# Kernel optimization log

Hardware: AMD Instinct MI355X
Metric: run time of the kernel (lower is better)

Reference implementation:

```python
import math
import jax, jax.numpy as jnp
import numpy as np

B, L, H, D = 1, 2048, 16, 64
M = 24            # nb_features
WINDOW = 128      # local_context / window_size
SCALE = 0.125     # softmax_scale = 1/sqrt(D)
MASK_VAL = -10000.0
EPS = 1e-4        # SBPerformerFeatures eps


def setup_inputs() -> dict:
    key = jax.random.key(0)
    k1, k2 = jax.random.split(key)
    qkv = jax.random.normal(k1, (B, L, 3, H, D), dtype=jnp.float32)
    proj = jax.random.normal(k2, (M, D), dtype=jnp.float32)  # Performer random features
    return {"qkv": qkv, "proj": proj}


def _performer_features(x, proj, is_query):
    # Softmax-kernel random features with separate log scale (scatterbrain SBPerformerFeatures).
    # exp(t*q.k) ~= exp(q_log + k_log) * <q_prime, k_prime>
    dn = math.sqrt(SCALE)
    xs = x * dn                                            # (b,h,l,d)
    x_dash = jnp.einsum('bhld,md->bhlm', xs, proj)         # (b,h,l,m)
    x_norm = 0.5 * jnp.sum(xs * xs, axis=-1, keepdims=True)
    half_log_m = 0.5 * math.log(M)
    if is_query:
        stab = jax.lax.stop_gradient(jnp.max(x_dash, axis=-1, keepdims=True))
        prime = jnp.exp(x_dash - stab) + EPS               # per-row stabilized
        log_scale = stab - x_norm - half_log_m             # (b,h,l,1)
    else:
        stab = jax.lax.stop_gradient(jnp.max(x_dash, axis=(-1, -2), keepdims=True))
        prime = jnp.exp(x_dash - x_norm - stab) + EPS      # norm folded in (needed for cumsum)
        log_scale = stab - half_log_m                      # (b,h,1,1)
    return prime, log_scale


def _band_mask(n):
    idx = jnp.arange(n)
    diff = idx[:, None] - idx[None, :]                     # i - j
    return jnp.where((diff >= 0) & (diff <= WINDOW), 0.0, MASK_VAL)  # (L,L)


def _forward(qkv, proj):
    q, k, v = qkv[:, :, 0], qkv[:, :, 1], qkv[:, :, 2]     # (b,l,h,d)
    q = jnp.transpose(q, (0, 2, 1, 3))                     # (b,h,l,d)
    k = jnp.transpose(k, (0, 2, 1, 3))
    v = jnp.transpose(v, (0, 2, 1, 3))

    # --- GlobalPerformer path ---
    q_prime, q_log = _performer_features(q, proj, True)    # (b,h,l,m), (b,h,l,1)
    k_prime, k_log = _performer_features(k, proj, False)   # (b,h,l,m), (b,h,1,1)
    global_scale = q_log + k_log                           # (b,h,l,1)

    k_cum = jnp.cumsum(k_prime, axis=2)
    global_out_cumsum = jnp.einsum('bhlm,bhlm->bhl', q_prime, k_cum)
    # causal_dot_product: out_i = q'_i . sum_{j<=i} k'_j v_j^T
    kv = jnp.cumsum(k_prime[..., :, None] * v[..., None, :], axis=2)   # (b,h,l,m,d)
    global_out = jnp.einsum('bhlm,bhlmd->bhld', q_prime, kv)

    mask = _band_mask(L)
    p_scores = jnp.einsum('bhme,bhne->bhmn', q_prime, k_prime) * SCALE
    global_qk = jnp.maximum(p_scores + mask[None, None], 0.0)  # masked_fill(<=0, 0)

    # --- Local exact softmax path ---
    scores = jnp.einsum('bhme,bhne->bhmn', q, k) * SCALE
    local_qk = scores + mask[None, None]
    qk_lse = jax.scipy.special.logsumexp(local_qk, axis=-1, keepdims=True)  # (b,h,l,1)

    gqk_sum = jnp.sum(global_qk, axis=-1, keepdims=True)
    global_log_norm = jnp.log(jnp.maximum(global_out_cumsum[..., None] - gqk_sum, 1e-24)) + global_scale
    log_norm = jnp.logaddexp(qk_lse, global_log_norm)      # (b,h,l,1)
    global_prime_scale = jnp.exp(global_scale - log_norm)  # (b,h,l,1)

    local_score = jax.nn.softmax(local_qk - log_norm, axis=-1) - global_qk * global_prime_scale
    out = jnp.einsum('bhmn,bhnd->bhmd', local_score, v) + global_out * global_prime_scale
    return jnp.transpose(out, (0, 2, 1, 3))                # (b,l,h,d)


def reference(qkv, proj):
    return _forward(qkv, proj)
```

## Files before the change

### kernel.cpp

```cpp
#include <hip/hip_runtime.h>
#include <hip/hip_bf16.h>

#define L_SEQ 2048
#define NH 16
#define DH 64
#define NCH 32
#define SCALE_F 0.125f
#define EPS_F 1e-4f
#define DN_F 0.35355339059327373f
#define HLM_F 1.5890269151739727f

typedef __attribute__((ext_vector_type(8))) short short8v;
typedef __attribute__((ext_vector_type(4))) float f32x4;

__device__ __forceinline__ unsigned short f2bf(float x) {
  unsigned u = __float_as_uint(x);
  u += 0x7FFFu + ((u >> 16) & 1u);
  return (unsigned short)(u >> 16);
}
__device__ __forceinline__ unsigned pk2(float a, float b) {
  return (unsigned)f2bf(a) | ((unsigned)f2bf(b) << 16);
}
__device__ __forceinline__ float stab_from_pmax(const float* __restrict__ pmax, int h, int t) {
  float v = pmax[h * 32 + (t & 31)];
  v = fmaxf(v, __shfl_xor(v, 1));  v = fmaxf(v, __shfl_xor(v, 2));
  v = fmaxf(v, __shfl_xor(v, 4));  v = fmaxf(v, __shfl_xor(v, 8));
  v = fmaxf(v, __shfl_xor(v, 16));
  return v;
}

__global__ __launch_bounds__(256) void k1_feat(
    const float* __restrict__ qkv, const float* __restrict__ proj,
    float* __restrict__ kdash, float* __restrict__ knorm,
    float* __restrict__ qdash, float* __restrict__ qnorm,
    float* __restrict__ pmax, unsigned* __restrict__ kbw, unsigned* __restrict__ qbw)
{
  __shared__ __attribute__((aligned(16))) float sP[24][68];
  __shared__ __attribute__((aligned(16))) float sX[64][68];
  __shared__ float sRed[256];
  const int c = blockIdx.x, h = blockIdx.y, qk = blockIdx.z, t = threadIdx.x;
  const int slot = qk ? 0 : 1;
  for (int i = t; i < 24 * 64; i += 256) sP[i >> 6][i & 63] = proj[i];
  for (int i = t; i < 1024; i += 256) {
    int rr = i >> 4, d4 = (i & 15) * 4;
    int l = c * 64 + rr;
    *(float4*)&sX[rr][d4] = *(const float4*)(qkv + (((size_t)l * 3 + slot) * NH + h) * DH + d4);
  }
  __syncthreads();
  unsigned* dstw = qk ? qbw : kbw;
  for (int w = t; w < 2048; w += 256) {
    int rr = w >> 5, wo = w & 31;
    int l = c * 64 + rr;
    float2 xv = *(const float2*)&sX[rr][2 * wo];
    dstw[((size_t)h * L_SEQ + l) * 32 + (wo ^ ((rr & 7) << 2))] = pk2(xv.x, xv.y);
  }
  const int r = t >> 2, mg = t & 3;
  float acc[6] = {0.f, 0.f, 0.f, 0.f, 0.f, 0.f};
  float sq = 0.f;
  for (int d4 = 0; d4 < 16; ++d4) {
    float4 xv = *(const float4*)&sX[r][d4 * 4];
    sq += xv.x * xv.x; sq += xv.y * xv.y; sq += xv.z * xv.z; sq += xv.w * xv.w;
#pragma unroll
    for (int i = 0; i < 6; ++i) {
      float4 pv = *(const float4*)&sP[mg * 6 + i][d4 * 4];
      acc[i] += xv.x * pv.x; acc[i] += xv.y * pv.y;
      acc[i] += xv.z * pv.z; acc[i] += xv.w * pv.w;
    }
  }
  int l = c * 64 + r;
  float* dsh = qk ? qdash : kdash;
  float lmax = -1e30f;
#pragma unroll
  for (int i = 0; i < 6; ++i) {
    float v = acc[i] * DN_F;
    dsh[((size_t)h * L_SEQ + l) * 24 + mg * 6 + i] = v;
    lmax = fmaxf(lmax, v);
  }
  if (mg == 0) (qk ? qnorm : knorm)[h * L_SEQ + l] = 0.5f * SCALE_F * sq;
  if (qk == 0) {
    sRed[t] = lmax;
    __syncthreads();
#pragma unroll
    for (int s = 128; s > 0; s >>= 1) {
      if (t < s) sRed[t] = fmaxf(sRed[t], sRed[t + s]);
      __syncthreads();
    }
    if (t == 0) pmax[h * 32 + c] = sRed[0];
  }
}

__global__ __launch_bounds__(256) void k3_kprime(
    const float* __restrict__ qkv, const float* __restrict__ kdash,
    const float* __restrict__ knorm, const float* __restrict__ pmax,
    unsigned* __restrict__ kpw, float* __restrict__ kpfx, float* __restrict__ kvs,
    unsigned* __restrict__ vtw)
{
  __shared__ float sKp[64][25];
  __shared__ __attribute__((aligned(16))) float sV[64][68];
  const int c = blockIdx.x, h = blockIdx.y, t = threadIdx.x;
  const float stab = stab_from_pmax(pmax, h, t);
  for (int i = t; i < 1024; i += 256) {
    int rr = i >> 4, d4 = (i & 15) * 4;
    int l = c * 64 + rr;
    *(float4*)&sV[rr][d4] = *(const float4*)(qkv + (((size_t)l * 3 + 2) * NH + h) * DH + d4);
  }
  for (int i = t; i < 1536; i += 256) {
    int r = i / 24, m = i % 24;
    int l = c * 64 + r;
    sKp[r][m] = __expf(kdash[((size_t)h * L_SEQ + l) * 24 + m] - knorm[h * L_SEQ + l] - stab) + EPS_F;
  }
  __syncthreads();
  for (int w = t; w < 1024; w += 256) {
    int r = w >> 4, wo = w & 15;
    int l = c * 64 + r;
    float a = (wo < 12) ? sKp[r][2 * wo] : 0.f;
    float bb = (wo < 12) ? sKp[r][2 * wo + 1] : 0.f;
    kpw[((size_t)h * L_SEQ + l) * 16 + (wo ^ ((r & 3) << 2))] = pk2(a, bb);
  }
  for (int w = t; w < 2048; w += 256) {
    int d = w >> 5, jp = w & 31;
    vtw[((size_t)h * NCH + c) * 2048 + d * 32 + (jp ^ ((d & 7) << 2))] = pk2(sV[2 * jp][d], sV[2 * jp + 1][d]);
  }
  if (t < 192) {
    const int m = t % 24, dO = (t / 24) * 8;
    float a0x = 0.f, a0y = 0.f, a0z = 0.f, a0w = 0.f;
    float a1x = 0.f, a1y = 0.f, a1z = 0.f, a1w = 0.f;
    for (int r2 = 0; r2 < 64; ++r2) {
      float kp = sKp[r2][m];
      float4 v0 = *(const float4*)&sV[r2][dO];
      float4 v1 = *(const float4*)&sV[r2][dO + 4];
      a0x += kp * v0.x; a0y += kp * v0.y; a0z += kp * v0.z; a0w += kp * v0.w;
      a1x += kp * v1.x; a1y += kp * v1.y; a1z += kp * v1.z; a1w += kp * v1.w;
    }
    float* dst = kvs + ((size_t)h * NCH + c) * 1536 + m * 64 + dO;
    float4 o0 = {a0x, a0y, a0z, a0w};
    float4 o1 = {a1x, a1y, a1z, a1w};
    *(float4*)dst = o0;
    *(float4*)(dst + 4) = o1;
  } else if (t < 216) {
    const int m = t - 192;
    float run = 0.f;
    for (int r2 = 0; r2 < 64; ++r2) {
      run += sKp[r2][m];
      kpfx[((size_t)h * L_SEQ + c * 64 + r2) * 24 + m] = run;
    }
  }
}

__global__ __launch_bounds__(256, 2) void k6_attn(
    const unsigned* __restrict__ kpw, const float* __restrict__ kpfx,
    const float* __restrict__ kvs, const unsigned* __restrict__ vtw,
    const float* __restrict__ qdash, const float* __restrict__ qnorm,
    const float* __restrict__ pmax, const unsigned* __restrict__ kbw,
    const unsigned* __restrict__ qbw, float* __restrict__ out)
{
  __shared__ __attribute__((aligned(16))) char lds[80736];
  char* sKW = lds;
  char* sKp = lds + 24576;
  char* sV  = lds + 36864;
  char* sQ  = lds + 61440;
  char* sQp = lds + 69632;
  float* sSum = (float*)(lds + 73728);
  float* sGps = sSum + 64;
  float* sRin = sGps + 64;
  float* sKcx = (float*)(lds + 74496);
  float* sPfx = (float*)(lds + 74592);

  const int b = blockIdx.x, h = blockIdx.y, t = threadIdx.x;
  const int wv = t >> 6, lane = t & 63, g = lane >> 4, ln = lane & 15;
  const int keybase = b * 64 - 128;
  const int jmin = (b >= 2) ? 0 : (128 - 64 * b);
  const int rA = wv * 16 + ln;

  for (int w = t; w < 1536; w += 256) {
    int r = w >> 3, q4 = w & 7;
    int l = keybase + r; l = l < 0 ? 0 : l;
    *(uint4*)(sKW + r * 128 + q4 * 16) = *(const uint4*)(kbw + ((size_t)h * L_SEQ + l) * 32 + q4 * 4);
  }
  for (int w = t; w < 512; w += 256) {
    int r = w >> 3, q4 = w & 7;
    int l = b * 64 + r;
    *(uint4*)(sQ + r * 128 + q4 * 16) = *(const uint4*)(qbw + ((size_t)h * L_SEQ + l) * 32 + q4 * 4);
  }
  for (int w = t; w < 768; w += 256) {
    int r = w >> 2, q4 = w & 3;
    int l = keybase + r; l = l < 0 ? 0 : l;
    *(uint4*)(sKp + r * 64 + q4 * 16) = *(const uint4*)(kpw + ((size_t)h * L_SEQ + l) * 16 + q4 * 4);
  }
  for (int w = t; w < 1536; w += 256) {
    int vt = w >> 9, idx = w & 511;
    int lt = b - 2 + vt; lt = lt < 0 ? 0 : lt;
    *(uint4*)(sV + vt * 8192 + idx * 16) = *(const uint4*)(vtw + ((size_t)h * NCH + lt) * 2048 + idx * 4);
  }
  const float stab = stab_from_pmax(pmax, h, t);
  {
    float accp[6] = {0.f, 0.f, 0.f, 0.f, 0.f, 0.f};
    const float* srcb = kvs + (size_t)h * NCH * 1536 + t;
    int bp = 0;
    for (; bp + 4 <= b; bp += 4) {
      float v0[6], v1[6], v2[6], v3[6];
#pragma unroll
      for (int j = 0; j < 6; ++j) v0[j] = srcb[(size_t)(bp + 0) * 1536 + j * 256];
#pragma unroll
      for (int j = 0; j < 6; ++j) v1[j] = srcb[(size_t)(bp + 1) * 1536 + j * 256];
#pragma unroll
      for (int j = 0; j < 6; ++j) v2[j] = srcb[(size_t)(bp + 2) * 1536 + j * 256];
#pragma unroll
      for (int j = 0; j < 6; ++j) v3[j] = srcb[(size_t)(bp + 3) * 1536 + j * 256];
#pragma unroll
      for (int j = 0; j < 6; ++j) {
        accp[j] += v0[j]; accp[j] += v1[j]; accp[j] += v2[j]; accp[j] += v3[j];
      }
    }
    for (; bp < b; ++bp) {
#pragma unroll
      for (int j = 0; j < 6; ++j) accp[j] += srcb[(size_t)bp * 1536 + j * 256];
    }
#pragma unroll
    for (int j = 0; j < 6; ++j) sPfx[t + j * 256] = accp[j];
  }
  if (t < 24) {
    float runk = 0.f;
    for (int bp = 0; bp < b; ++bp)
      runk += kpfx[((size_t)h * L_SEQ + bp * 64 + 63) * 24 + t];
    sKcx[t] = runk;
  }
  float qlog = 0.f;
  float qpv[24];
  if (t < 64) {
    int r = t, l = b * 64 + r;
    const float* qdp = qdash + ((size_t)h * L_SEQ + l) * 24;
    float qd[24];
#pragma unroll
    for (int i = 0; i < 6; ++i) {
      float4 v = *(const float4*)(qdp + 4 * i);
      qd[4 * i] = v.x; qd[4 * i + 1] = v.y; qd[4 * i + 2] = v.z; qd[4 * i + 3] = v.w;
    }
    float mx = -1e30f;
#pragma unroll
    for (int m = 0; m < 24; ++m) mx = fmaxf(mx, qd[m]);
#pragma unroll
    for (int m = 0; m < 24; ++m) qpv[m] = __expf(qd[m] - mx) + EPS_F;
    qlog = mx - qnorm[h * L_SEQ + l] - HLM_F;
#pragma unroll
    for (int wo = 0; wo < 16; ++wo) {
      float a = (wo < 12) ? qpv[2 * wo] : 0.f;
      float bb = (wo < 12) ? qpv[2 * wo + 1] : 0.f;
      *(unsigned*)(sQp + (r * 64 + (((wo * 4)) ^ ((r & 3) << 4)))) = pk2(a, bb);
    }
  }
  __syncthreads();

  float eF[12][4];
  float rs[4] = {0.f, 0.f, 0.f, 0.f};
  short8v aS0 = *(const short8v*)(sQ + (rA * 128 + ((g * 16) ^ ((rA & 7) << 4))));
  short8v aS1 = *(const short8v*)(sQ + (rA * 128 + ((64 + g * 16) ^ ((rA & 7) << 4))));
#pragma unroll
  for (int nt = 0; nt < 12; ++nt) {
    int rB = nt * 16 + ln;
    short8v b0 = *(const short8v*)(sKW + (rB * 128 + ((g * 16) ^ ((rB & 7) << 4))));
    short8v b1 = *(const short8v*)(sKW + (rB * 128 + ((64 + g * 16) ^ ((rB & 7) << 4))));
    f32x4 acc = {0.f, 0.f, 0.f, 0.f};
    acc = __builtin_amdgcn_mfma_f32_16x16x32_bf16(aS0, b0, acc, 0, 0, 0);
    acc = __builtin_amdgcn_mfma_f32_16x16x32_bf16(aS1, b1, acc, 0, 0, 0);
    int j = nt * 16 + ln;
#pragma unroll
    for (int reg = 0; reg < 4; ++reg) {
      int rl = wv * 16 + g * 4 + reg;
      float e = 0.f;
      if (j >= rl && j <= rl + 128 && j >= jmin) e = __expf(SCALE_F * acc[reg]);
      eF[nt][reg] = e;
      rs[reg] += e;
    }
  }
#pragma unroll
  for (int reg = 0; reg < 4; ++reg) {
    float v = rs[reg];
    v += __shfl_xor(v, 1); v += __shfl_xor(v, 2);
    v += __shfl_xor(v, 4); v += __shfl_xor(v, 8);
    if (ln == 0) sSum[wv * 16 + g * 4 + reg] = v;
  }

  float pF[12][4];
  short8v aP = *(const short8v*)(sQp + (rA * 64 + ((g * 16) ^ ((rA & 3) << 4))));
#pragma unroll
  for (int nt = 0; nt < 12; ++nt) {
    int rB = nt * 16 + ln;
    short8v bp = *(const short8v*)(sKp + (rB * 64 + ((g * 16) ^ ((rB & 3) << 4))));
    f32x4 acc = {0.f, 0.f, 0.f, 0.f};
    acc = __builtin_amdgcn_mfma_f32_16x16x32_bf16(aP, bp, acc, 0, 0, 0);
#pragma unroll
    for (int reg = 0; reg < 4; ++reg) pF[nt][reg] = acc[reg];
  }
  __syncthreads();

  if (t < 64) {
    int r = t, l = b * 64 + r;
    const float* kfc = kpfx + ((size_t)h * L_SEQ + l) * 24;
    int b1i = (b >= 1) ? b - 1 : 0;
    int b2i = (b >= 2) ? b - 2 : 0;
    int rm1 = (r >= 1) ? r - 1 : 0;
    const float* T1p = kpfx + ((size_t)h * L_SEQ + b1i * 64 + 63) * 24;
    const float* T2p = kpfx + ((size_t)h * L_SEQ + b2i * 64 + 63) * 24;
    const float* S2p = kpfx + ((size_t)h * L_SEQ + b2i * 64 + rm1) * 24;
    float f1 = (b >= 1) ? 1.f : 0.f;
    float f2 = (b >= 2) ? 1.f : 0.f;
    float fr = (b >= 2 && r >= 1) ? 1.f : 0.f;
    float psc = 0.f, kcs = 0.f, bnd = 0.f;
#pragma unroll
    for (int m = 0; m < 24; ++m) {
      float qp = qpv[m];
      float kc = kfc[m];
      psc += qp * kc;
      kcs += qp * sKcx[m];
      bnd += qp * (kc + f1 * T1p[m] + f2 * T2p[m] - fr * S2p[m]);
    }
    float goc = kcs + psc;
    float gqk = SCALE_F * bnd;
    float se = sSum[r];
    float lse = __logf(se);
    float gscale = qlog + stab - HLM_F;
    float gln = __logf(fmaxf(goc - gqk, 1e-24f)) + gscale;
    float mx2 = fmaxf(lse, gln), mn2 = fminf(lse, gln);
    float lognorm = mx2 + log1pf(__expf(mn2 - mx2));
    sGps[r] = __expf(gscale - lognorm);
    sRin[r] = 1.f / se;
  }
  __syncthreads();

  float gpr[4], rin[4];
#pragma unroll
  for (int reg = 0; reg < 4; ++reg) {
    int rl = wv * 16 + g * 4 + reg;
    gpr[reg] = sGps[rl];
    rin[reg] = sRin[rl];
  }
#pragma unroll
  for (int nt = 0; nt < 12; ++nt) {
    int j = nt * 16 + ln;
#pragma unroll
    for (int reg = 0; reg < 4; ++reg) {
      int rl = wv * 16 + g * 4 + reg;
      bool causal = (j >= 128) && (j <= 128 + rl);
      bool bprev = (j >= rl) && (j < 128) && (j >= jmin);
      float coef = causal ? (1.f - SCALE_F) * gpr[reg] : (bprev ? -SCALE_F * gpr[reg] : 0.f);
      float wgt = eF[nt][reg] * rin[reg] + coef * pF[nt][reg];
      float wn = __shfl_xor(wgt, 1);
      if ((ln & 1) == 0) {
        *(unsigned*)(sKW + (rl * 384 + ((j * 2) ^ ((rl & 7) << 4)))) = pk2(wgt, wn);
      }
    }
  }
  __syncthreads();

  for (int w = t; w < 1024; w += 256) {
    int d = w >> 4, mp = w & 15;
    int m0 = 2 * mp, m1 = m0 + 1;
    float a = (m0 < 24) ? sPfx[m0 * 64 + d] : 0.f;
    float bb = (m1 < 24) ? sPfx[m1 * 64 + d] : 0.f;
    *(unsigned*)(sKp + (d * 64 + ((mp * 4) ^ ((d & 3) << 4)))) = pk2(a, bb);
  }

  f32x4 oF[4];
#pragma unroll
  for (int dt = 0; dt < 4; ++dt) { f32x4 z = {0.f, 0.f, 0.f, 0.f}; oF[dt] = z; }
#pragma unroll
  for (int vt3 = 0; vt3 < 3; ++vt3) {
    const char* vbase = sV + vt3 * 8192;
#pragma unroll
    for (int ks = 0; ks < 2; ++ks) {
      short8v aw = *(const short8v*)(sKW + (rA * 384 + ((vt3 * 128 + ks * 64 + g * 16) ^ ((rA & 7) << 4))));
#pragma unroll
      for (int dt = 0; dt < 4; ++dt) {
        int rB = dt * 16 + ln;
        short8v bv = *(const short8v*)(vbase + (rB * 128 + ((ks * 64 + g * 16) ^ ((rB & 7) << 4))));
        oF[dt] = __builtin_amdgcn_mfma_f32_16x16x32_bf16(aw, bv, oF[dt], 0, 0, 0);
      }
    }
  }
  __syncthreads();

  short8v aq = *(const short8v*)(sQp + (rA * 64 + ((g * 16) ^ ((rA & 3) << 4))));
  f32x4 ogF[4];
#pragma unroll
  for (int dt = 0; dt < 4; ++dt) {
    int rB = dt * 16 + ln;
    short8v bg = *(const short8v*)(sKp + (rB * 64 + ((g * 16) ^ ((rB & 3) << 4))));
    f32x4 z = {0.f, 0.f, 0.f, 0.f};
    ogF[dt] = __builtin_amdgcn_mfma_f32_16x16x32_bf16(aq, bg, z, 0, 0, 0);
  }

#pragma unroll
  for (int dt = 0; dt < 4; ++dt) {
    int d = dt * 16 + ln;
#pragma unroll
    for (int reg = 0; reg < 4; ++reg) {
      int rl = wv * 16 + g * 4 + reg;
      int l = b * 64 + rl;
      out[((size_t)l * NH + h) * DH + d] = oF[dt][reg] + gpr[reg] * ogF[dt][reg];
    }
  }
}

extern "C" void kernel_launch(void* const* d_in, const int* in_sizes, int n_in,
                              void* d_out, int out_size, void* d_ws, size_t ws_size,
                              hipStream_t stream)
{
  const float* qkv = (const float*)d_in[0];
  const float* proj = (const float*)d_in[1];
  float* out = (float*)d_out;
  char* ws = (char*)d_ws;

  float* kdash   = (float*)(ws + 0);
  float* qdash   = (float*)(ws + 3145728);
  float* knorm   = (float*)(ws + 6291456);
  float* qnorm   = (float*)(ws + 6422528);
  float* pmax    = (float*)(ws + 6553600);
  unsigned* kbw  = (unsigned*)(ws + 6555648);
  unsigned* qbw  = (unsigned*)(ws + 10749952);
  unsigned* kpw  = (unsigned*)(ws + 14944256);
  float* kpfx    = (float*)(ws + 17041408);
  unsigned* vtw  = (unsigned*)(ws + 20187136);
  float* kvs     = (float*)(ws + 24381440);

  k1_feat<<<dim3(NCH, NH, 2), 256, 0, stream>>>(qkv, proj, kdash, knorm, qdash, qnorm, pmax, kbw, qbw);
  k3_kprime<<<dim3(NCH, NH), 256, 0, stream>>>(qkv, kdash, knorm, pmax, kpw, kpfx, kvs, vtw);
  k6_attn<<<dim3(NCH, NH), 256, 0, stream>>>(kpw, kpfx, kvs, vtw, qdash, qnorm, pmax, kbw, qbw, out);
}
```

Measured before the change: 120.0 us.

## Fuse feature and k-prime kernels via per-chunk max with deferred global rescale

Merges the two preprocessing kernels into one. It computes k features relative to a per-chunk max, so they no longer depend on the global per-head max, and it also precomputes the q primes, their log scales and a packed q-prime layout. The attention kernel then rescales the chunk partial sums, prefix sums and key tiles by exp(chunkmax - globalmax) and adds the EPS contributions analytically, using extra per-chunk v sums. This removes one launch and the kdash/qdash round trip through global memory, at the cost of extra exp and fma work and additional loads in the attention kernel.

```diff
diff --git a/kernel.cpp b/kernel.cpp
--- a/kernel.cpp
+++ b/kernel.cpp
@@ -29,32 +29,34 @@
   return v;
 }
 
-__global__ __launch_bounds__(256) void k1_feat(
+__global__ __launch_bounds__(256) void k0_feat(
     const float* __restrict__ qkv, const float* __restrict__ proj,
-    float* __restrict__ kdash, float* __restrict__ knorm,
-    float* __restrict__ qdash, float* __restrict__ qnorm,
-    float* __restrict__ pmax, unsigned* __restrict__ kbw, unsigned* __restrict__ qbw)
+    float* __restrict__ pmax, unsigned* __restrict__ kbw, unsigned* __restrict__ qbw,
+    unsigned* __restrict__ qpw, float* __restrict__ qpv_g, float* __restrict__ qlog_g,
+    float* __restrict__ a_g, float* __restrict__ apfx_g, float* __restrict__ avs_g,
+    unsigned* __restrict__ vtw)
 {
   __shared__ __attribute__((aligned(16))) float sP[24][68];
   __shared__ __attribute__((aligned(16))) float sX[64][68];
+  __shared__ float sA[64][25];
   __shared__ float sRed[256];
-  const int c = blockIdx.x, h = blockIdx.y, qk = blockIdx.z, t = threadIdx.x;
-  const int slot = qk ? 0 : 1;
-  for (int i = t; i < 24 * 64; i += 256) sP[i >> 6][i & 63] = proj[i];
+  const int c = blockIdx.x, h = blockIdx.y, t = threadIdx.x;
+  const int r = t >> 2, mg = t & 3;
+  const int l0 = c * 64 + r;
+  for (int i = t; i < 1536; i += 256) sP[i >> 6][i & 63] = proj[i];
+
   for (int i = t; i < 1024; i += 256) {
     int rr = i >> 4, d4 = (i & 15) * 4;
     int l = c * 64 + rr;
-    *(float4*)&sX[rr][d4] = *(const float4*)(qkv + (((size_t)l * 3 + slot) * NH + h) * DH + d4);
-  }
-  __syncthreads();
-  unsigned* dstw = qk ? qbw : kbw;
+    *(float4*)&sX[rr][d4] = *(const float4*)(qkv + (((size_t)l * 3 + 1) * NH + h) * DH + d4);
+  }
+  __syncthreads();
   for (int w = t; w < 2048; w += 256) {
     int rr = w >> 5, wo = w & 31;
     int l = c * 64 + rr;
     float2 xv = *(const float2*)&sX[rr][2 * wo];
-    dstw[((size_t)h * L_SEQ + l) * 32 + (wo ^ ((rr & 7) << 2))] = pk2(xv.x, xv.y);
-  }
-  const int r = t >> 2, mg = t & 3;
+    kbw[((size_t)h * L_SEQ + l) * 32 + (wo ^ ((rr & 7) << 2))] = pk2(xv.x, xv.y);
+  }
   float acc[6] = {0.f, 0.f, 0.f, 0.f, 0.f, 0.f};
   float sq = 0.f;
   for (int d4 = 0; d4 < 16; ++d4) {
@@ -67,110 +69,141 @@
       acc[i] += xv.z * pv.z; acc[i] += xv.w * pv.w;
     }
   }
-  int l = c * 64 + r;
-  float* dsh = qk ? qdash : kdash;
-  float lmax = -1e30f;
+  float kd[6]; float lmax = -1e30f;
+#pragma unroll
+  for (int i = 0; i < 6; ++i) { kd[i] = acc[i] * DN_F; lmax = fmaxf(lmax, kd[i]); }
+  const float kn = 0.5f * SCALE_F * sq;
+  sRed[t] = lmax;
+  __syncthreads();
+#pragma unroll
+  for (int s = 128; s > 0; s >>= 1) {
+    if (t < s) sRed[t] = fmaxf(sRed[t], sRed[t + s]);
+    __syncthreads();
+  }
+  const float cmax = sRed[0];
+  if (t == 0) pmax[h * 32 + c] = cmax;
 #pragma unroll
   for (int i = 0; i < 6; ++i) {
-    float v = acc[i] * DN_F;
-    dsh[((size_t)h * L_SEQ + l) * 24 + mg * 6 + i] = v;
-    lmax = fmaxf(lmax, v);
-  }
-  if (mg == 0) (qk ? qnorm : knorm)[h * L_SEQ + l] = 0.5f * SCALE_F * sq;
-  if (qk == 0) {
-    sRed[t] = lmax;
-    __syncthreads();
-#pragma unroll
-    for (int s = 128; s > 0; s >>= 1) {
-      if (t < s) sRed[t] = fmaxf(sRed[t], sRed[t + s]);
-      __syncthreads();
-    }
-    if (t == 0) pmax[h * 32 + c] = sRed[0];
-  }
-}
-
-__global__ __launch_bounds__(256) void k3_kprime(
-    const float* __restrict__ qkv, const float* __restrict__ kdash,
-    const float* __restrict__ knorm, const float* __restrict__ pmax,
-    unsigned* __restrict__ kpw, float* __restrict__ kpfx, float* __restrict__ kvs,
-    unsigned* __restrict__ vtw)
-{
-  __shared__ float sKp[64][25];
-  __shared__ __attribute__((aligned(16))) float sV[64][68];
-  const int c = blockIdx.x, h = blockIdx.y, t = threadIdx.x;
-  const float stab = stab_from_pmax(pmax, h, t);
+    float av = __expf(kd[i] - kn - cmax);
+    sA[r][mg * 6 + i] = av;
+    a_g[((size_t)h * L_SEQ + l0) * 24 + mg * 6 + i] = av;
+  }
+
   for (int i = t; i < 1024; i += 256) {
     int rr = i >> 4, d4 = (i & 15) * 4;
     int l = c * 64 + rr;
-    *(float4*)&sV[rr][d4] = *(const float4*)(qkv + (((size_t)l * 3 + 2) * NH + h) * DH + d4);
-  }
-  for (int i = t; i < 1536; i += 256) {
-    int r = i / 24, m = i % 24;
-    int l = c * 64 + r;
-    sKp[r][m] = __expf(kdash[((size_t)h * L_SEQ + l) * 24 + m] - knorm[h * L_SEQ + l] - stab) + EPS_F;
-  }
-  __syncthreads();
-  for (int w = t; w < 1024; w += 256) {
-    int r = w >> 4, wo = w & 15;
-    int l = c * 64 + r;
-    float a = (wo < 12) ? sKp[r][2 * wo] : 0.f;
-    float bb = (wo < 12) ? sKp[r][2 * wo + 1] : 0.f;
-    kpw[((size_t)h * L_SEQ + l) * 16 + (wo ^ ((r & 3) << 2))] = pk2(a, bb);
-  }
+    *(float4*)&sX[rr][d4] = *(const float4*)(qkv + (((size_t)l * 3 + 0) * NH + h) * DH + d4);
+  }
+  __syncthreads();
+  for (int w = t; w < 2048; w += 256) {
+    int rr = w >> 5, wo = w & 31;
+    int l = c * 64 + rr;
+    float2 xv = *(const float2*)&sX[rr][2 * wo];
+    qbw[((size_t)h * L_SEQ + l) * 32 + (wo ^ ((rr & 7) << 2))] = pk2(xv.x, xv.y);
+  }
+  float qacc[6] = {0.f, 0.f, 0.f, 0.f, 0.f, 0.f};
+  float qsq = 0.f;
+  for (int d4 = 0; d4 < 16; ++d4) {
+    float4 xv = *(const float4*)&sX[r][d4 * 4];
+    qsq += xv.x * xv.x; qsq += xv.y * xv.y; qsq += xv.z * xv.z; qsq += xv.w * xv.w;
+#pragma unroll
+    for (int i = 0; i < 6; ++i) {
+      float4 pv = *(const float4*)&sP[mg * 6 + i][d4 * 4];
+      qacc[i] += xv.x * pv.x; qacc[i] += xv.y * pv.y;
+      qacc[i] += xv.z * pv.z; qacc[i] += xv.w * pv.w;
+    }
+  }
+  float qd6[6]; float qmx = -1e30f;
+#pragma unroll
+  for (int i = 0; i < 6; ++i) { qd6[i] = qacc[i] * DN_F; qmx = fmaxf(qmx, qd6[i]); }
+  qmx = fmaxf(qmx, __shfl_xor(qmx, 1));
+  qmx = fmaxf(qmx, __shfl_xor(qmx, 2));
+  float qp6[6];
+#pragma unroll
+  for (int i = 0; i < 6; ++i) {
+    qp6[i] = __expf(qd6[i] - qmx) + EPS_F;
+    qpv_g[((size_t)h * L_SEQ + l0) * 24 + mg * 6 + i] = qp6[i];
+  }
+#pragma unroll
+  for (int j = 0; j < 3; ++j)
+    qpw[((size_t)h * L_SEQ + l0) * 16 + ((3 * mg + j) ^ ((r & 3) << 2))] = pk2(qp6[2 * j], qp6[2 * j + 1]);
+  if (mg == 0) {
+#pragma unroll
+    for (int j = 0; j < 4; ++j)
+      qpw[((size_t)h * L_SEQ + l0) * 16 + ((12 + j) ^ ((r & 3) << 2))] = 0u;
+    qlog_g[(size_t)h * L_SEQ + l0] = qmx - 0.5f * SCALE_F * qsq - HLM_F;
+  }
+
+  __syncthreads();
+  for (int i = t; i < 1024; i += 256) {
+    int rr = i >> 4, d4 = (i & 15) * 4;
+    int l = c * 64 + rr;
+    *(float4*)&sX[rr][d4] = *(const float4*)(qkv + (((size_t)l * 3 + 2) * NH + h) * DH + d4);
+  }
+  __syncthreads();
   for (int w = t; w < 2048; w += 256) {
     int d = w >> 5, jp = w & 31;
-    vtw[((size_t)h * NCH + c) * 2048 + d * 32 + (jp ^ ((d & 7) << 2))] = pk2(sV[2 * jp][d], sV[2 * jp + 1][d]);
+    vtw[((size_t)h * NCH + c) * 2048 + d * 32 + (jp ^ ((d & 7) << 2))] = pk2(sX[2 * jp][d], sX[2 * jp + 1][d]);
   }
   if (t < 192) {
     const int m = t % 24, dO = (t / 24) * 8;
     float a0x = 0.f, a0y = 0.f, a0z = 0.f, a0w = 0.f;
     float a1x = 0.f, a1y = 0.f, a1z = 0.f, a1w = 0.f;
     for (int r2 = 0; r2 < 64; ++r2) {
-      float kp = sKp[r2][m];
-      float4 v0 = *(const float4*)&sV[r2][dO];
-      float4 v1 = *(const float4*)&sV[r2][dO + 4];
+      float kp = sA[r2][m];
+      float4 v0 = *(const float4*)&sX[r2][dO];
+      float4 v1 = *(const float4*)&sX[r2][dO + 4];
       a0x += kp * v0.x; a0y += kp * v0.y; a0z += kp * v0.z; a0w += kp * v0.w;
       a1x += kp * v1.x; a1y += kp * v1.y; a1z += kp * v1.z; a1w += kp * v1.w;
     }
-    float* dst = kvs + ((size_t)h * NCH + c) * 1536 + m * 64 + dO;
+    float* dst = avs_g + ((size_t)h * NCH + c) * 1600 + m * 64 + dO;
     float4 o0 = {a0x, a0y, a0z, a0w};
     float4 o1 = {a1x, a1y, a1z, a1w};
     *(float4*)dst = o0;
     *(float4*)(dst + 4) = o1;
-  } else if (t < 216) {
-    const int m = t - 192;
-    float run = 0.f;
-    for (int r2 = 0; r2 < 64; ++r2) {
-      run += sKp[r2][m];
-      kpfx[((size_t)h * L_SEQ + c * 64 + r2) * 24 + m] = run;
-    }
+  } else {
+    int m = t - 192;
+    if (m < 24) {
+      float run = 0.f;
+      for (int r2 = 0; r2 < 64; ++r2) {
+        run += sA[r2][m];
+        apfx_g[((size_t)h * L_SEQ + c * 64 + r2) * 24 + m] = run;
+      }
+    }
+    int d = t - 192;
+    float vs = 0.f;
+    for (int r2 = 0; r2 < 64; ++r2) vs += sX[r2][d];
+    avs_g[((size_t)h * NCH + c) * 1600 + 1536 + d] = vs;
   }
 }
 
 __global__ __launch_bounds__(256, 2) void k6_attn(
-    const unsigned* __restrict__ kpw, const float* __restrict__ kpfx,
-    const float* __restrict__ kvs, const unsigned* __restrict__ vtw,
-    const float* __restrict__ qdash, const float* __restrict__ qnorm,
     const float* __restrict__ pmax, const unsigned* __restrict__ kbw,
-    const unsigned* __restrict__ qbw, float* __restrict__ out)
+    const unsigned* __restrict__ qbw, const unsigned* __restrict__ qpw,
+    const float* __restrict__ qpv_g, const float* __restrict__ qlog_g,
+    const float* __restrict__ a_g, const float* __restrict__ apfx_g,
+    const float* __restrict__ avs_g, const unsigned* __restrict__ vtw,
+    float* __restrict__ out)
 {
-  __shared__ __attribute__((aligned(16))) char lds[80736];
+  __shared__ __attribute__((aligned(16))) char lds[80992];
   char* sKW = lds;
   char* sKp = lds + 24576;
   char* sV  = lds + 36864;
   char* sQ  = lds + 61440;
   char* sQp = lds + 69632;
   float* sSum = (float*)(lds + 73728);
-  float* sGps = sSum + 64;
-  float* sRin = sGps + 64;
+  float* sGps = (float*)(lds + 73984);
+  float* sRin = (float*)(lds + 74240);
   float* sKcx = (float*)(lds + 74496);
-  float* sPfx = (float*)(lds + 74592);
+  float* sVx  = (float*)(lds + 74592);
+  float* sPfx = (float*)(lds + 74848);
 
   const int b = blockIdx.x, h = blockIdx.y, t = threadIdx.x;
   const int wv = t >> 6, lane = t & 63, g = lane >> 4, ln = lane & 15;
   const int keybase = b * 64 - 128;
   const int jmin = (b >= 2) ? 0 : (128 - 64 * b);
   const int rA = wv * 16 + ln;
+  const float stab = stab_from_pmax(pmax, h, t);
 
   for (int w = t; w < 1536; w += 256) {
     int r = w >> 3, q4 = w & 7;
@@ -182,72 +215,91 @@
     int l = b * 64 + r;
     *(uint4*)(sQ + r * 128 + q4 * 16) = *(const uint4*)(qbw + ((size_t)h * L_SEQ + l) * 32 + q4 * 4);
   }
-  for (int w = t; w < 768; w += 256) {
+  for (int w = t; w < 256; w += 256) {
     int r = w >> 2, q4 = w & 3;
-    int l = keybase + r; l = l < 0 ? 0 : l;
-    *(uint4*)(sKp + r * 64 + q4 * 16) = *(const uint4*)(kpw + ((size_t)h * L_SEQ + l) * 16 + q4 * 4);
+    int l = b * 64 + r;
+    *(uint4*)(sQp + r * 64 + q4 * 16) = *(const uint4*)(qpw + ((size_t)h * L_SEQ + l) * 16 + q4 * 4);
   }
   for (int w = t; w < 1536; w += 256) {
     int vt = w >> 9, idx = w & 511;
     int lt = b - 2 + vt; lt = lt < 0 ? 0 : lt;
     *(uint4*)(sV + vt * 8192 + idx * 16) = *(const uint4*)(vtw + ((size_t)h * NCH + lt) * 2048 + idx * 4);
   }
-  const float stab = stab_from_pmax(pmax, h, t);
+  for (int w = t; w < 2304; w += 256) {
+    int r = w / 12, p = w % 12;
+    int l = keybase + r; l = l < 0 ? 0 : l;
+    float s = __expf(pmax[h * 32 + (l >> 6)] - stab);
+    const float* ap = a_g + ((size_t)h * L_SEQ + l) * 24 + 2 * p;
+    float k0v = fmaf(s, ap[0], EPS_F);
+    float k1v = fmaf(s, ap[1], EPS_F);
+    *(unsigned*)(sKp + (r * 64 + 4 * (p ^ ((r & 3) << 2)))) = pk2(k0v, k1v);
+  }
+  for (int w = t; w < 768; w += 256) {
+    int r = w >> 2, p = 12 + (w & 3);
+    *(unsigned*)(sKp + (r * 64 + 4 * (p ^ ((r & 3) << 2)))) = 0u;
+  }
   {
     float accp[6] = {0.f, 0.f, 0.f, 0.f, 0.f, 0.f};
-    const float* srcb = kvs + (size_t)h * NCH * 1536 + t;
+    float vexc = 0.f;
+    const float* srcb = avs_g + (size_t)h * NCH * 1600;
     int bp = 0;
     for (; bp + 4 <= b; bp += 4) {
+      float s0 = __expf(pmax[h * 32 + bp + 0] - stab);
+      float s1 = __expf(pmax[h * 32 + bp + 1] - stab);
+      float s2 = __expf(pmax[h * 32 + bp + 2] - stab);
+      float s3 = __expf(pmax[h * 32 + bp + 3] - stab);
       float v0[6], v1[6], v2[6], v3[6];
 #pragma unroll
-      for (int j = 0; j < 6; ++j) v0[j] = srcb[(size_t)(bp + 0) * 1536 + j * 256];
-#pragma unroll
-      for (int j = 0; j < 6; ++j) v1[j] = srcb[(size_t)(bp + 1) * 1536 + j * 256];
-#pragma unroll
-      for (int j = 0; j < 6; ++j) v2[j] = srcb[(size_t)(bp + 2) * 1536 + j * 256];
-#pragma unroll
-      for (int j = 0; j < 6; ++j) v3[j] = srcb[(size_t)(bp + 3) * 1536 + j * 256];
+      for (int j = 0; j < 6; ++j) v0[j] = srcb[(size_t)(bp + 0) * 1600 + t + j * 256];
+#pragma unroll
+      for (int j = 0; j < 6; ++j) v1[j] = srcb[(size_t)(bp + 1) * 1600 + t + j * 256];
+#pragma unroll
+      for (int j = 0; j < 6; ++j) v2[j] = srcb[(size_t)(bp + 2) * 1600 + t + j * 256];
+#pragma unroll
+      for (int j = 0; j < 6; ++j) v3[j] = srcb[(size_t)(bp + 3) * 1600 + t + j * 256];
+      float w0 = 0.f, w1 = 0.f, w2 = 0.f, w3 = 0.f;
+      if (t < 64) {
+        w0 = srcb[(size_t)(bp + 0) * 1600 + 1536 + t];
+        w1 = srcb[(size_t)(bp + 1) * 1600 + 1536 + t];
+        w2 = srcb[(size_t)(bp + 2) * 1600 + 1536 + t];
+        w3 = srcb[(size_t)(bp + 3) * 1600 + 1536 + t];
+      }
 #pragma unroll
       for (int j = 0; j < 6; ++j) {
-        accp[j] += v0[j]; accp[j] += v1[j]; accp[j] += v2[j]; accp[j] += v3[j];
+        accp[j] = fmaf(s0, v0[j], accp[j]); accp[j] = fmaf(s1, v1[j], accp[j]);
+        accp[j] = fmaf(s2, v2[j], accp[j]); accp[j] = fmaf(s3, v3[j], accp[j]);
       }
+      if (t < 64) { vexc += w0; vexc += w1; vexc += w2; vexc += w3; }
     }
     for (; bp < b; ++bp) {
-#pragma unroll
-      for (int j = 0; j < 6; ++j) accp[j] += srcb[(size_t)bp * 1536 + j * 256];
+      float s = __expf(pmax[h * 32 + bp] - stab);
+#pragma unroll
+      for (int j = 0; j < 6; ++j) accp[j] = fmaf(s, srcb[(size_t)bp * 1600 + t + j * 256], accp[j]);
+      if (t < 64) vexc += srcb[(size_t)bp * 1600 + 1536 + t];
     }
 #pragma unroll
     for (int j = 0; j < 6; ++j) sPfx[t + j * 256] = accp[j];
+    if (t < 64) sVx[t] = vexc;
   }
   if (t < 24) {
     float runk = 0.f;
-    for (int bp = 0; bp < b; ++bp)
-      runk += kpfx[((size_t)h * L_SEQ + bp * 64 + 63) * 24 + t];
-    sKcx[t] = runk;
+    for (int bp = 0; bp < b; ++bp) {
+      float s = __expf(pmax[h * 32 + bp] - stab);
+      runk = fmaf(s, apfx_g[((size_t)h * L_SEQ + bp * 64 + 63) * 24 + t], runk);
+    }
+    sKcx[t] = runk + EPS_F * 64.f * (float)b;
   }
   float qlog = 0.f;
   float qpv[24];
   if (t < 64) {
-    int r = t, l = b * 64 + r;
-    const float* qdp = qdash + ((size_t)h * L_SEQ + l) * 24;
-    float qd[24];
+    int l = b * 64 + t;
+    const float* qdp = qpv_g + ((size_t)h * L_SEQ + l) * 24;
 #pragma unroll
     for (int i = 0; i < 6; ++i) {
       float4 v = *(const float4*)(qdp + 4 * i);
-      qd[4 * i] = v.x; qd[4 * i + 1] = v.y; qd[4 * i + 2] = v.z; qd[4 * i + 3] = v.w;
-    }
-    float mx = -1e30f;
-#pragma unroll
-    for (int m = 0; m < 24; ++m) mx = fmaxf(mx, qd[m]);
-#pragma unroll
-    for (int m = 0; m < 24; ++m) qpv[m] = __expf(qd[m] - mx) + EPS_F;
-    qlog = mx - qnorm[h * L_SEQ + l] - HLM_F;
-#pragma unroll
-    for (int wo = 0; wo < 16; ++wo) {
-      float a = (wo < 12) ? qpv[2 * wo] : 0.f;
-      float bb = (wo < 12) ? qpv[2 * wo + 1] : 0.f;
-      *(unsigned*)(sQp + (r * 64 + (((wo * 4)) ^ ((r & 3) << 4)))) = pk2(a, bb);
-    }
+      qpv[4 * i] = v.x; qpv[4 * i + 1] = v.y; qpv[4 * i + 2] = v.z; qpv[4 * i + 3] = v.w;
+    }
+    qlog = qlog_g[(size_t)h * L_SEQ + l];
   }
   __syncthreads();
 
@@ -296,24 +348,31 @@
 
   if (t < 64) {
     int r = t, l = b * 64 + r;
-    const float* kfc = kpfx + ((size_t)h * L_SEQ + l) * 24;
+    const float* apO = apfx_g + ((size_t)h * L_SEQ + l) * 24;
     int b1i = (b >= 1) ? b - 1 : 0;
     int b2i = (b >= 2) ? b - 2 : 0;
     int rm1 = (r >= 1) ? r - 1 : 0;
-    const float* T1p = kpfx + ((size_t)h * L_SEQ + b1i * 64 + 63) * 24;
-    const float* T2p = kpfx + ((size_t)h * L_SEQ + b2i * 64 + 63) * 24;
-    const float* S2p = kpfx + ((size_t)h * L_SEQ + b2i * 64 + rm1) * 24;
+    const float* T1a = apfx_g + ((size_t)h * L_SEQ + b1i * 64 + 63) * 24;
+    const float* T2a = apfx_g + ((size_t)h * L_SEQ + b2i * 64 + 63) * 24;
+    const float* S2a = apfx_g + ((size_t)h * L_SEQ + b2i * 64 + rm1) * 24;
     float f1 = (b >= 1) ? 1.f : 0.f;
     float f2 = (b >= 2) ? 1.f : 0.f;
     float fr = (b >= 2 && r >= 1) ? 1.f : 0.f;
+    float sb = __expf(pmax[h * 32 + b] - stab);
+    float s1 = __expf(pmax[h * 32 + b1i] - stab);
+    float s2 = __expf(pmax[h * 32 + b2i] - stab);
+    float cEr = EPS_F * (float)(r + 1), cE64 = EPS_F * 64.f, cEr1 = EPS_F * (float)(rm1 + 1);
     float psc = 0.f, kcs = 0.f, bnd = 0.f;
 #pragma unroll
     for (int m = 0; m < 24; ++m) {
       float qp = qpv[m];
-      float kc = kfc[m];
+      float kc  = fmaf(sb, apO[m], cEr);
+      float t1v = fmaf(s1, T1a[m], cE64);
+      float t2v = fmaf(s2, T2a[m], cE64);
+      float s2v = fmaf(s2, S2a[m], cEr1);
       psc += qp * kc;
       kcs += qp * sKcx[m];
-      bnd += qp * (kc + f1 * T1p[m] + f2 * T2p[m] - fr * S2p[m]);
+      bnd += qp * (kc + f1 * t1v + f2 * t2v - fr * s2v);
     }
     float goc = kcs + psc;
     float gqk = SCALE_F * bnd;
@@ -356,8 +415,9 @@
   for (int w = t; w < 1024; w += 256) {
     int d = w >> 4, mp = w & 15;
     int m0 = 2 * mp, m1 = m0 + 1;
-    float a = (m0 < 24) ? sPfx[m0 * 64 + d] : 0.f;
-    float bb = (m1 < 24) ? sPfx[m1 * 64 + d] : 0.f;
+    float base = EPS_F * sVx[d];
+    float a = (m0 < 24) ? sPfx[m0 * 64 + d] + base : 0.f;
+    float bb = (m1 < 24) ? sPfx[m1 * 64 + d] + base : 0.f;
     *(unsigned*)(sKp + (d * 64 + ((mp * 4) ^ ((d & 3) << 4)))) = pk2(a, bb);
   }
 
@@ -411,19 +471,19 @@
   float* out = (float*)d_out;
   char* ws = (char*)d_ws;
 
-  float* kdash   = (float*)(ws + 0);
-  float* qdash   = (float*)(ws + 3145728);
-  float* knorm   = (float*)(ws + 6291456);
-  float* qnorm   = (float*)(ws + 6422528);
-  float* pmax    = (float*)(ws + 6553600);
-  unsigned* kbw  = (unsigned*)(ws + 6555648);
-  unsigned* qbw  = (unsigned*)(ws + 10749952);
-  unsigned* kpw  = (unsigned*)(ws + 14944256);
-  float* kpfx    = (float*)(ws + 17041408);
-  unsigned* vtw  = (unsigned*)(ws + 20187136);
-  float* kvs     = (float*)(ws + 24381440);
-
-  k1_feat<<<dim3(NCH, NH, 2), 256, 0, stream>>>(qkv, proj, kdash, knorm, qdash, qnorm, pmax, kbw, qbw);
-  k3_kprime<<<dim3(NCH, NH), 256, 0, stream>>>(qkv, kdash, knorm, pmax, kpw, kpfx, kvs, vtw);
-  k6_attn<<<dim3(NCH, NH), 256, 0, stream>>>(kpw, kpfx, kvs, vtw, qdash, qnorm, pmax, kbw, qbw, out);
-}
+  float* pmax    = (float*)(ws + 0);
+  unsigned* kbw  = (unsigned*)(ws + 4096);
+  unsigned* qbw  = (unsigned*)(ws + 4198400);
+  unsigned* qpw  = (unsigned*)(ws + 8392704);
+  float* qpv_g   = (float*)(ws + 10489856);
+  float* qlog_g  = (float*)(ws + 13635584);
+  float* a_g     = (float*)(ws + 13766656);
+  float* apfx_g  = (float*)(ws + 16912384);
+  float* avs_g   = (float*)(ws + 20058112);
+  unsigned* vtw  = (unsigned*)(ws + 23334912);
+
+  k0_feat<<<dim3(NCH, NH), 256, 0, stream>>>(qkv, proj, pmax, kbw, qbw, qpw,
+                                             qpv_g, qlog_g, a_g, apfx_g, avs_g, vtw);
+  k6_attn<<<dim3(NCH, NH), 256, 0, stream>>>(pmax, kbw, qbw, qpw, qpv_g, qlog_g,
+                                             a_g, apfx_g, avs_g, vtw, out);
+}
```

Result: faster. 117.5 us (-2.0%).
